# Performance work log

Measured on AMD Instinct MI355X. Metric: run time of the kernel, lower is better.

The kernel has to match this reference:

```python
import jax, jax.numpy as jnp
import numpy as np

D_MODEL = 768
N_HEAD = 8
D_K = D_MODEL // N_HEAD
SCALE = float(np.sqrt(D_K))
NEG = -1e9


def setup_inputs() -> dict:
    key = jax.random.key(0)
    ks = jax.random.split(key, 8)
    B, S = 2, 2048
    q = jax.random.normal(ks[0], (B, S, D_MODEL), dtype=jnp.float32)
    k = jax.random.normal(ks[1], (B, S, D_MODEL), dtype=jnp.float32)
    v = jax.random.normal(ks[2], (B, S, D_MODEL), dtype=jnp.float32)
    mask = jax.random.randint(ks[3], (B, 1, S, S), 0, 2, dtype=jnp.int32)
    # nn.Linear(d, d, bias=False) weights, stored as [in, out] for x @ W
    init = 1.0 / np.sqrt(D_MODEL)
    Wq = jax.random.uniform(ks[4], (D_MODEL, D_MODEL), jnp.float32, -init, init)
    Wk = jax.random.uniform(ks[5], (D_MODEL, D_MODEL), jnp.float32, -init, init)
    Wv = jax.random.uniform(ks[6], (D_MODEL, D_MODEL), jnp.float32, -init, init)
    Wo = jax.random.uniform(ks[7], (D_MODEL, D_MODEL), jnp.float32, -init, init)
    return {"query": q, "key": k, "value": v, "mask": mask,
            "Wq": Wq, "Wk": Wk, "Wv": Wv, "Wo": Wo}


def _split_heads(x):
    B, S, _ = x.shape
    return x.reshape(B, S, N_HEAD, D_K).transpose(0, 2, 1, 3)  # [B,H,S,Dk]


def reference(query, key, value, mask, Wq, Wk, Wv, Wo):
    Q = _split_heads(query @ Wq)
    K = _split_heads(key @ Wk)
    V = _split_heads(value @ Wv)
    logits = jnp.einsum('bhqd,bhkd->bhqk', Q, K) / SCALE  # [B,H,S,S]
    logits = jnp.where(mask == 0, NEG, logits)
    attn = jax.nn.softmax(logits, axis=-1)
    x = jnp.einsum('bhqk,bhkd->bhqd', attn, V)  # dropout=0 (eval)
    B, H, S, Dk = x.shape
    concat = x.transpose(0, 2, 1, 3).reshape(B, S, H * Dk)
    return concat @ Wo, attn
```

## Files before the change

### kernel.cpp

```cpp
#include <hip/hip_runtime.h>
#include <hip/hip_bf16.h>

typedef __bf16 bf16_t;
typedef __bf16 bf16x4 __attribute__((ext_vector_type(4)));
typedef __bf16 bf16x8 __attribute__((ext_vector_type(8)));
typedef float f32x4 __attribute__((ext_vector_type(4)));

#define MFMA16(a, b, c) __builtin_amdgcn_mfma_f32_16x16x32_bf16(a, b, c, 0, 0, 0)

constexpr int B_ = 2, S_ = 2048, DM = 768, H_ = 8, DK = 96;
constexpr size_t OUT_ELEMS = 3145728;
constexpr float INV_SCALE = 0.10206207261596575f;
constexpr float NEGINF = -1e9f;


__global__ __launch_bounds__(256) void prep_w(const float* __restrict__ w0,
                                              const float* __restrict__ w1,
                                              const float* __restrict__ w2,
                                              const float* __restrict__ w3,
                                              bf16_t* __restrict__ wt) {
    __shared__ float tile[32][33];
    const int z = blockIdx.z;
    const float* W = (z == 0) ? w0 : (z == 1) ? w1 : (z == 2) ? w2 : w3;
    bf16_t* out = wt + (size_t)z * DM * DM;
    const int k0 = blockIdx.x * 32, n0 = blockIdx.y * 32;
    const int tx = threadIdx.x & 31, ty = threadIdx.x >> 5;
#pragma unroll
    for (int i = 0; i < 32; i += 8) tile[ty + i][tx] = W[(size_t)(k0 + ty + i) * DM + n0 + tx];
    __syncthreads();
#pragma unroll
    for (int i = 0; i < 32; i += 8) out[(size_t)(n0 + ty + i) * DM + k0 + tx] = (bf16_t)tile[tx][ty + i];
}

template <int AMODE>
__device__ __forceinline__ void gemm_core(const void* __restrict__ Aglob,
                                          const bf16_t* __restrict__ Bt,
                                          int gm0, int gn0, f32x4 acc[4][4]) {
    __shared__ bf16_t As[128][40];
    __shared__ bf16_t Bs[128][40];
    const int tid = threadIdx.x, lane = tid & 63, wid = tid >> 6;
    const int wr = wid >> 1, wc = wid & 1;
    const int l15 = lane & 15, lq = lane >> 4;
    for (int kt = 0; kt < DM / 32; ++kt) {
        if (AMODE == 0) {
            const float* A = (const float*)Aglob;
#pragma unroll
            for (int p = 0; p < 4; ++p) {
                const int row = p * 32 + (tid >> 3);
                const int c4 = (tid & 7) * 4;
                const float4 vv = *(const float4*)&A[(size_t)(gm0 + row) * DM + kt * 32 + c4];
                As[row][c4 + 0] = (bf16_t)vv.x; As[row][c4 + 1] = (bf16_t)vv.y;
                As[row][c4 + 2] = (bf16_t)vv.z; As[row][c4 + 3] = (bf16_t)vv.w;
            }
        } else {
            const bf16_t* A = (const bf16_t*)Aglob;
#pragma unroll
            for (int p = 0; p < 2; ++p) {
                const int row = p * 64 + (tid >> 2);
                const int c8 = (tid & 3) * 8;
                *(uint4*)&As[row][c8] = *(const uint4*)&A[(size_t)(gm0 + row) * DM + kt * 32 + c8];
            }
        }
#pragma unroll
        for (int p = 0; p < 2; ++p) {
            const int row = p * 64 + (tid >> 2);
            const int c8 = (tid & 3) * 8;
            *(uint4*)&Bs[row][c8] = *(const uint4*)&Bt[(size_t)(gn0 + row) * DM + kt * 32 + c8];
        }
        __syncthreads();
        bf16x8 af[4], bfr[4];
#pragma unroll
        for (int i = 0; i < 4; ++i) af[i] = *(const bf16x8*)&As[wr * 64 + i * 16 + l15][lq * 8];
#pragma unroll
        for (int i = 0; i < 4; ++i) bfr[i] = *(const bf16x8*)&Bs[wc * 64 + i * 16 + l15][lq * 8];
#pragma unroll
        for (int i = 0; i < 4; ++i)
#pragma unroll
            for (int j = 0; j < 4; ++j) acc[i][j] = MFMA16(af[i], bfr[j], acc[i][j]);
        __syncthreads();
    }
}

__global__ __launch_bounds__(256) void qkv_gemm(const float* __restrict__ Xq,
                                                const float* __restrict__ Xk,
                                                const float* __restrict__ Xv,
                                                const bf16_t* __restrict__ Wt,
                                                bf16_t* __restrict__ Qw,
                                                bf16_t* __restrict__ Kw,
                                                bf16_t* __restrict__ Vt) {
    const int z = blockIdx.z;
    const float* A = (z == 0) ? Xq : (z == 1) ? Xk : Xv;
    const bf16_t* Bz = Wt + (size_t)z * DM * DM;
    const int gm0 = blockIdx.x * 128, gn0 = blockIdx.y * 128;
    f32x4 acc[4][4];
#pragma unroll
    for (int i = 0; i < 4; ++i)
#pragma unroll
        for (int j = 0; j < 4; ++j) acc[i][j] = (f32x4){0.f, 0.f, 0.f, 0.f};
    gemm_core<0>(A, Bz, gm0, gn0, acc);
    const int lane = threadIdx.x & 63, wid = threadIdx.x >> 6;
    const int wr = wid >> 1, wc = wid & 1;
#pragma unroll
    for (int i = 0; i < 4; ++i)
#pragma unroll
        for (int j = 0; j < 4; ++j)
#pragma unroll
            for (int e = 0; e < 4; ++e) {
                const int gm = gm0 + wr * 64 + i * 16 + (lane >> 4) * 4 + e;
                const int gn = gn0 + wc * 64 + j * 16 + (lane & 15);
                const int b = gm >> 11, s = gm & 2047;
                const int h = gn / DK, dk = gn % DK;
                const float val = acc[i][j][e];
                if (z == 2)
                    Vt[(((size_t)b * H_ + h) * DK + dk) * S_ + s] = (bf16_t)val;
                else {
                    bf16_t* dst = (z == 0) ? Qw : Kw;
                    dst[(((size_t)b * H_ + h) * S_ + s) * DK + dk] = (bf16_t)val;
                }
            }
}

__global__ __launch_bounds__(256, 1) void attn_fused(const bf16_t* __restrict__ Qw,
                                                     const bf16_t* __restrict__ Kw,
                                                     const int* __restrict__ mask,
                                                     const bf16_t* __restrict__ Vt,
                                                     float* __restrict__ attnf,
                                                     bf16_t* __restrict__ Xc) {
    const int bh = blockIdx.y;
    const int q0 = blockIdx.x * 16;
    const int tid = threadIdx.x, lane = tid & 63, w = tid >> 6;
    const int l15 = lane & 15, lq = lane >> 4;
    const int b = bh >> 3, h = bh & 7;

    __shared__ float redmax[4][16];
    __shared__ float redsum[4][16];
    __shared__ bf16_t p_lds[4][16][40];
    __shared__ float pv_part[4][16][96];

    bf16x8 aq[3];
    const bf16_t* qbase = Qw + ((size_t)bh * S_ + q0 + l15) * DK + lq * 8;
#pragma unroll
    for (int kk = 0; kk < 3; ++kk) aq[kk] = *(const bf16x8*)(qbase + kk * 32);

    f32x4 accs[32];
    float rmax = -1e30f;
    const bf16_t* kbase = Kw + (size_t)bh * S_ * DK;
    const int* mrow = mask + ((size_t)b * S_ + q0 + l15) * S_;

#pragma unroll
    for (int t = 0; t < 32; ++t) {
        const int c0 = (w * 32 + t) * 16;
        f32x4 acc = {0.f, 0.f, 0.f, 0.f};
#pragma unroll
        for (int kk = 0; kk < 3; ++kk) {
            bf16x8 kf = *(const bf16x8*)(kbase + (size_t)(c0 + l15) * DK + kk * 32 + lq * 8);
            acc = MFMA16(kf, aq[kk], acc);
        }
        const int4 mk = *(const int4*)(mrow + c0 + lq * 4);
        const int mke[4] = {mk.x, mk.y, mk.z, mk.w};
#pragma unroll
        for (int e = 0; e < 4; ++e) {
            const float lv = (mke[e] == 0) ? NEGINF : acc[e] * INV_SCALE;
            acc[e] = lv;
            rmax = fmaxf(rmax, lv);
        }
        accs[t] = acc;
    }
    rmax = fmaxf(rmax, __shfl_xor(rmax, 16, 64));
    rmax = fmaxf(rmax, __shfl_xor(rmax, 32, 64));
    if (lane < 16) redmax[w][lane] = rmax;
    __syncthreads();
    const float gmax = fmaxf(fmaxf(redmax[0][l15], redmax[1][l15]),
                             fmaxf(redmax[2][l15], redmax[3][l15]));

    float rsum = 0.f;
#pragma unroll
    for (int t = 0; t < 32; ++t) {
#pragma unroll
        for (int e = 0; e < 4; ++e) {
            const float ev = __expf(accs[t][e] - gmax);
            accs[t][e] = ev;
            rsum += ev;
        }
    }
    rsum += __shfl_xor(rsum, 16, 64);
    rsum += __shfl_xor(rsum, 32, 64);
    if (lane < 16) redsum[w][lane] = rsum;
    __syncthreads();
    const float inv = 1.0f / (redsum[0][l15] + redsum[1][l15] + redsum[2][l15] + redsum[3][l15]);

    f32x4 acc6[6];
#pragma unroll
    for (int f = 0; f < 6; ++f) acc6[f] = (f32x4){0.f, 0.f, 0.f, 0.f};
    float* arow = attnf + ((size_t)bh * S_ + q0 + l15) * S_;
    const bf16_t* vbase = Vt + (size_t)bh * DK * S_ + lq * 8;

    for (int u = 0; u < 16; ++u) {
#pragma unroll
        for (int half = 0; half < 2; ++half) {
            const int t = 2 * u + half;
            const int c0 = (w * 32 + t) * 16;
            bf16x4 nb;
#pragma unroll
            for (int e = 0; e < 4; ++e) nb[e] = (bf16_t)(accs[t][e] * inv);
            float4 st;
            st.x = (float)nb[0]; st.y = (float)nb[1]; st.z = (float)nb[2]; st.w = (float)nb[3];
            *(float4*)(arow + c0 + lq * 4) = st;
            *(bf16x4*)&p_lds[w][l15][half * 16 + lq * 4] = nb;
        }
        asm volatile("s_waitcnt lgkmcnt(0)" ::: "memory");
        const bf16x8 pa = *(const bf16x8*)&p_lds[w][l15][lq * 8];
        const int k0 = (w * 512) + u * 32;
#pragma unroll
        for (int f = 0; f < 6; ++f) {
            const bf16x8 vb = *(const bf16x8*)(vbase + (size_t)(f * 16 + l15) * S_ + k0);
            acc6[f] = MFMA16(pa, vb, acc6[f]);
        }
    }

#pragma unroll
    for (int f = 0; f < 6; ++f)
#pragma unroll
        for (int e = 0; e < 4; ++e) pv_part[w][lq * 4 + e][f * 16 + l15] = acc6[f][e];
    __syncthreads();
    for (int i = tid; i < 16 * 96; i += 256) {
        const int row = i / 96, col = i % 96;
        const float s = pv_part[0][row][col] + pv_part[1][row][col] + pv_part[2][row][col] +
                        pv_part[3][row][col];
        Xc[((size_t)b * S_ + q0 + row) * DM + h * DK + col] = (bf16_t)s;
    }
}

__global__ __launch_bounds__(256) void out_gemm(const bf16_t* __restrict__ Xc,
                                                const bf16_t* __restrict__ Wot,
                                                float* __restrict__ outf) {
    const int gm0 = blockIdx.x * 128, gn0 = blockIdx.y * 128;
    f32x4 acc[4][4];
#pragma unroll
    for (int i = 0; i < 4; ++i)
#pragma unroll
        for (int j = 0; j < 4; ++j) acc[i][j] = (f32x4){0.f, 0.f, 0.f, 0.f};
    gemm_core<1>(Xc, Wot, gm0, gn0, acc);
    const int lane = threadIdx.x & 63, wid = threadIdx.x >> 6;
    const int wr = wid >> 1, wc = wid & 1;
#pragma unroll
    for (int i = 0; i < 4; ++i)
#pragma unroll
        for (int j = 0; j < 4; ++j)
#pragma unroll
            for (int e = 0; e < 4; ++e) {
                const int gm = gm0 + wr * 64 + i * 16 + (lane >> 4) * 4 + e;
                const int gn = gn0 + wc * 64 + j * 16 + (lane & 15);
                outf[(size_t)gm * DM + gn] = (float)(bf16_t)acc[i][j][e];
            }
}

extern "C" void kernel_launch(void* const* d_in, const int* in_sizes, int n_in,
                              void* d_out, int out_size, void* d_ws, size_t ws_size,
                              hipStream_t stream) {
    const float* q = (const float*)d_in[0];
    const float* k = (const float*)d_in[1];
    const float* v = (const float*)d_in[2];
    const int* mask = (const int*)d_in[3];
    const float* Wq = (const float*)d_in[4];
    const float* Wk = (const float*)d_in[5];
    const float* Wv = (const float*)d_in[6];
    const float* Wo = (const float*)d_in[7];

    float* outf = (float*)d_out;
    float* attnf = (float*)d_out + OUT_ELEMS;

    char* ws = (char*)d_ws;
    bf16_t* Qw = (bf16_t*)ws;
    bf16_t* Kw = Qw + (size_t)B_ * H_ * S_ * DK;
    bf16_t* Vt = Kw + (size_t)B_ * H_ * S_ * DK;
    bf16_t* Wt = Vt + (size_t)B_ * H_ * S_ * DK;
    bf16_t* Xc = Qw;

    Xc = Wt + (size_t)4 * DM * DM;

    prep_w<<<dim3(24, 24, 4), 256, 0, stream>>>(Wq, Wk, Wv, Wo, Wt);
    qkv_gemm<<<dim3(32, 6, 3), 256, 0, stream>>>(q, k, v, Wt, Qw, Kw, Vt);
    attn_fused<<<dim3(128, 16), 256, 0, stream>>>(Qw, Kw, mask, Vt, attnf, Xc);
    out_gemm<<<dim3(32, 6), 256, 0, stream>>>(Xc, Wt + (size_t)3 * DM * DM, outf);
}
```

Baseline: 260.4 us.

## Pack mask to bits and restructure attention into two-pass online softmax per wave

Result: slower. 316.1 us (+21.4%).

```diff
diff --git a/kernel.cpp b/kernel.cpp
--- a/kernel.cpp
+++ b/kernel.cpp
@@ -5,6 +5,7 @@
 typedef __bf16 bf16x4 __attribute__((ext_vector_type(4)));
 typedef __bf16 bf16x8 __attribute__((ext_vector_type(8)));
 typedef float f32x4 __attribute__((ext_vector_type(4)));
+typedef unsigned long long u64;
 
 #define MFMA16(a, b, c) __builtin_amdgcn_mfma_f32_16x16x32_bf16(a, b, c, 0, 0, 0)
 
@@ -13,6 +14,21 @@
 constexpr float INV_SCALE = 0.10206207261596575f;
 constexpr float NEGINF = -1e9f;
 
+constexpr size_t QW_OFF = 0, KW_OFF = 6291456, VT_OFF = 12582912, WT_OFF = 18874368;
+constexpr size_t XC_OFF = 23592960, MB_OFF = 29884416;
+
+__global__ __launch_bounds__(256) void pack_mask(const int* __restrict__ mask,
+                                                 u64* __restrict__ bits) {
+    const int row = blockIdx.x;
+    const int tid = threadIdx.x, lane = tid & 63, wv = tid >> 6;
+    const int* mrow = mask + (size_t)row * S_;
+    u64* brow = bits + (size_t)row * 32;
+#pragma unroll
+    for (int p = 0; p < 8; ++p) {
+        const u64 b = __ballot(mrow[p * 256 + wv * 64 + lane] != 0);
+        if (lane == 0) brow[p * 4 + wv] = b;
+    }
+}
 
 __global__ __launch_bounds__(256) void prep_w(const float* __restrict__ w0,
                                               const float* __restrict__ w1,
@@ -120,115 +136,146 @@
             }
 }
 
-__global__ __launch_bounds__(256, 1) void attn_fused(const bf16_t* __restrict__ Qw,
+__global__ __launch_bounds__(256, 4) void attn_fused(const bf16_t* __restrict__ Qw,
                                                      const bf16_t* __restrict__ Kw,
-                                                     const int* __restrict__ mask,
+                                                     const u64* __restrict__ mbits,
                                                      const bf16_t* __restrict__ Vt,
                                                      float* __restrict__ attnf,
                                                      bf16_t* __restrict__ Xc) {
     const int bh = blockIdx.y;
-    const int q0 = blockIdx.x * 16;
     const int tid = threadIdx.x, lane = tid & 63, w = tid >> 6;
     const int l15 = lane & 15, lq = lane >> 4;
     const int b = bh >> 3, h = bh & 7;
-
-    __shared__ float redmax[4][16];
-    __shared__ float redsum[4][16];
-    __shared__ bf16_t p_lds[4][16][40];
-    __shared__ float pv_part[4][16][96];
-
-    bf16x8 aq[3];
-    const bf16_t* qbase = Qw + ((size_t)bh * S_ + q0 + l15) * DK + lq * 8;
-#pragma unroll
-    for (int kk = 0; kk < 3; ++kk) aq[kk] = *(const bf16x8*)(qbase + kk * 32);
-
-    f32x4 accs[32];
-    float rmax = -1e30f;
-    const bf16_t* kbase = Kw + (size_t)bh * S_ * DK;
-    const int* mrow = mask + ((size_t)b * S_ + q0 + l15) * S_;
-
-#pragma unroll
-    for (int t = 0; t < 32; ++t) {
-        const int c0 = (w * 32 + t) * 16;
-        f32x4 acc = {0.f, 0.f, 0.f, 0.f};
+    const int qb = blockIdx.x * 128 + w * 32;
+
+    __shared__ bf16_t p_lds[4][2][16][40];
+
+    bf16x8 aq0[3], aq1[3];
+    {
+        const bf16_t* qb0 = Qw + ((size_t)bh * S_ + qb + l15) * DK + lq * 8;
+        const bf16_t* qb1 = qb0 + (size_t)16 * DK;
 #pragma unroll
         for (int kk = 0; kk < 3; ++kk) {
-            bf16x8 kf = *(const bf16x8*)(kbase + (size_t)(c0 + l15) * DK + kk * 32 + lq * 8);
-            acc = MFMA16(kf, aq[kk], acc);
-        }
-        const int4 mk = *(const int4*)(mrow + c0 + lq * 4);
-        const int mke[4] = {mk.x, mk.y, mk.z, mk.w};
+            aq0[kk] = *(const bf16x8*)(qb0 + kk * 32);
+            aq1[kk] = *(const bf16x8*)(qb1 + kk * 32);
+        }
+    }
+    const bf16_t* kbase = Kw + (size_t)bh * S_ * DK + lq * 8;
+    const u64* mb0 = mbits + ((size_t)b * S_ + qb + l15) * 32;
+    const u64* mb1 = mb0 + 16 * 32;
+
+    float m0 = -3e38f, s0 = 0.f, m1 = -3e38f, s1 = 0.f;
+    for (int tg = 0; tg < 32; ++tg) {
+        const u64 w0 = mb0[tg];
+        const u64 w1 = mb1[tg];
+#pragma unroll
+        for (int dt = 0; dt < 4; ++dt) {
+            const int t = tg * 4 + dt;
+            const bf16_t* kr = kbase + (size_t)(t * 16 + l15) * DK;
+            bf16x8 kf0 = *(const bf16x8*)(kr);
+            bf16x8 kf1 = *(const bf16x8*)(kr + 32);
+            bf16x8 kf2 = *(const bf16x8*)(kr + 64);
+            f32x4 a0 = {0.f, 0.f, 0.f, 0.f}, a1 = {0.f, 0.f, 0.f, 0.f};
+            a0 = MFMA16(kf0, aq0[0], a0); a0 = MFMA16(kf1, aq0[1], a0); a0 = MFMA16(kf2, aq0[2], a0);
+            a1 = MFMA16(kf0, aq1[0], a1); a1 = MFMA16(kf1, aq1[1], a1); a1 = MFMA16(kf2, aq1[2], a1);
+            const int sh = dt * 16 + lq * 4;
+            const unsigned b0 = (unsigned)(w0 >> sh) & 0xFu;
+            const unsigned b1 = (unsigned)(w1 >> sh) & 0xFu;
+            float lv0[4], lv1[4];
+#pragma unroll
+            for (int e = 0; e < 4; ++e) {
+                lv0[e] = ((b0 >> e) & 1u) ? a0[e] * INV_SCALE : NEGINF;
+                lv1[e] = ((b1 >> e) & 1u) ? a1[e] * INV_SCALE : NEGINF;
+            }
+            const float tm0 = fmaxf(fmaxf(lv0[0], lv0[1]), fmaxf(lv0[2], lv0[3]));
+            const float tm1 = fmaxf(fmaxf(lv1[0], lv1[1]), fmaxf(lv1[2], lv1[3]));
+            if (tm0 > m0) { s0 *= __expf(m0 - tm0); m0 = tm0; }
+            if (tm1 > m1) { s1 *= __expf(m1 - tm1); m1 = tm1; }
+#pragma unroll
+            for (int e = 0; e < 4; ++e) {
+                s0 += __expf(lv0[e] - m0);
+                s1 += __expf(lv1[e] - m1);
+            }
+        }
+    }
+#pragma unroll
+    for (int off = 16; off <= 32; off <<= 1) {
+        const float om0 = __shfl_xor(m0, off, 64), os0 = __shfl_xor(s0, off, 64);
+        const float om1 = __shfl_xor(m1, off, 64), os1 = __shfl_xor(s1, off, 64);
+        const float nm0 = fmaxf(m0, om0), nm1 = fmaxf(m1, om1);
+        s0 = s0 * __expf(m0 - nm0) + os0 * __expf(om0 - nm0);
+        s1 = s1 * __expf(m1 - nm1) + os1 * __expf(om1 - nm1);
+        m0 = nm0; m1 = nm1;
+    }
+    const float inv0 = 1.0f / s0, inv1 = 1.0f / s1;
+
+    f32x4 acc60[6], acc61[6];
+#pragma unroll
+    for (int f = 0; f < 6; ++f) {
+        acc60[f] = (f32x4){0.f, 0.f, 0.f, 0.f};
+        acc61[f] = (f32x4){0.f, 0.f, 0.f, 0.f};
+    }
+    float* arow0 = attnf + ((size_t)bh * S_ + qb + l15) * S_;
+    float* arow1 = arow0 + (size_t)16 * S_;
+    const bf16_t* vbase = Vt + (size_t)bh * DK * S_ + lq * 8;
+
+    for (int ug = 0; ug < 32; ++ug) {
+        const u64 w0 = mb0[ug];
+        const u64 w1 = mb1[ug];
+#pragma unroll
+        for (int uh = 0; uh < 2; ++uh) {
+            const int u = ug * 2 + uh;
+#pragma unroll
+            for (int half = 0; half < 2; ++half) {
+                const int t = u * 2 + half;
+                const bf16_t* kr = kbase + (size_t)(t * 16 + l15) * DK;
+                bf16x8 kf0 = *(const bf16x8*)(kr);
+                bf16x8 kf1 = *(const bf16x8*)(kr + 32);
+                bf16x8 kf2 = *(const bf16x8*)(kr + 64);
+                f32x4 a0 = {0.f, 0.f, 0.f, 0.f}, a1 = {0.f, 0.f, 0.f, 0.f};
+                a0 = MFMA16(kf0, aq0[0], a0); a0 = MFMA16(kf1, aq0[1], a0); a0 = MFMA16(kf2, aq0[2], a0);
+                a1 = MFMA16(kf0, aq1[0], a1); a1 = MFMA16(kf1, aq1[1], a1); a1 = MFMA16(kf2, aq1[2], a1);
+                const int sh = (uh * 2 + half) * 16 + lq * 4;
+                const unsigned b0 = (unsigned)(w0 >> sh) & 0xFu;
+                const unsigned b1 = (unsigned)(w1 >> sh) & 0xFu;
+                bf16x4 nb0, nb1;
+#pragma unroll
+                for (int e = 0; e < 4; ++e) {
+                    const float lv0 = ((b0 >> e) & 1u) ? a0[e] * INV_SCALE : NEGINF;
+                    const float lv1 = ((b1 >> e) & 1u) ? a1[e] * INV_SCALE : NEGINF;
+                    nb0[e] = (bf16_t)(__expf(lv0 - m0) * inv0);
+                    nb1[e] = (bf16_t)(__expf(lv1 - m1) * inv1);
+                }
+                float4 st0, st1;
+                st0.x = (float)nb0[0]; st0.y = (float)nb0[1]; st0.z = (float)nb0[2]; st0.w = (float)nb0[3];
+                st1.x = (float)nb1[0]; st1.y = (float)nb1[1]; st1.z = (float)nb1[2]; st1.w = (float)nb1[3];
+                *(float4*)(arow0 + t * 16 + lq * 4) = st0;
+                *(float4*)(arow1 + t * 16 + lq * 4) = st1;
+                *(bf16x4*)&p_lds[w][0][l15][half * 16 + lq * 4] = nb0;
+                *(bf16x4*)&p_lds[w][1][l15][half * 16 + lq * 4] = nb1;
+            }
+            asm volatile("s_waitcnt lgkmcnt(0)" ::: "memory");
+            const bf16x8 pa0 = *(const bf16x8*)&p_lds[w][0][l15][lq * 8];
+            const bf16x8 pa1 = *(const bf16x8*)&p_lds[w][1][l15][lq * 8];
+            const int k0 = u * 32;
+#pragma unroll
+            for (int f = 0; f < 6; ++f) {
+                const bf16x8 vb = *(const bf16x8*)(vbase + (size_t)(f * 16 + l15) * S_ + k0);
+                acc60[f] = MFMA16(pa0, vb, acc60[f]);
+                acc61[f] = MFMA16(pa1, vb, acc61[f]);
+            }
+        }
+    }
+
+#pragma unroll
+    for (int f = 0; f < 6; ++f)
 #pragma unroll
         for (int e = 0; e < 4; ++e) {
-            const float lv = (mke[e] == 0) ? NEGINF : acc[e] * INV_SCALE;
-            acc[e] = lv;
-            rmax = fmaxf(rmax, lv);
-        }
-        accs[t] = acc;
-    }
-    rmax = fmaxf(rmax, __shfl_xor(rmax, 16, 64));
-    rmax = fmaxf(rmax, __shfl_xor(rmax, 32, 64));
-    if (lane < 16) redmax[w][lane] = rmax;
-    __syncthreads();
-    const float gmax = fmaxf(fmaxf(redmax[0][l15], redmax[1][l15]),
-                             fmaxf(redmax[2][l15], redmax[3][l15]));
-
-    float rsum = 0.f;
-#pragma unroll
-    for (int t = 0; t < 32; ++t) {
-#pragma unroll
-        for (int e = 0; e < 4; ++e) {
-            const float ev = __expf(accs[t][e] - gmax);
-            accs[t][e] = ev;
-            rsum += ev;
-        }
-    }
-    rsum += __shfl_xor(rsum, 16, 64);
-    rsum += __shfl_xor(rsum, 32, 64);
-    if (lane < 16) redsum[w][lane] = rsum;
-    __syncthreads();
-    const float inv = 1.0f / (redsum[0][l15] + redsum[1][l15] + redsum[2][l15] + redsum[3][l15]);
-
-    f32x4 acc6[6];
-#pragma unroll
-    for (int f = 0; f < 6; ++f) acc6[f] = (f32x4){0.f, 0.f, 0.f, 0.f};
-    float* arow = attnf + ((size_t)bh * S_ + q0 + l15) * S_;
-    const bf16_t* vbase = Vt + (size_t)bh * DK * S_ + lq * 8;
-
-    for (int u = 0; u < 16; ++u) {
-#pragma unroll
-        for (int half = 0; half < 2; ++half) {
-            const int t = 2 * u + half;
-            const int c0 = (w * 32 + t) * 16;
-            bf16x4 nb;
-#pragma unroll
-            for (int e = 0; e < 4; ++e) nb[e] = (bf16_t)(accs[t][e] * inv);
-            float4 st;
-            st.x = (float)nb[0]; st.y = (float)nb[1]; st.z = (float)nb[2]; st.w = (float)nb[3];
-            *(float4*)(arow + c0 + lq * 4) = st;
-            *(bf16x4*)&p_lds[w][l15][half * 16 + lq * 4] = nb;
-        }
-        asm volatile("s_waitcnt lgkmcnt(0)" ::: "memory");
-        const bf16x8 pa = *(const bf16x8*)&p_lds[w][l15][lq * 8];
-        const int k0 = (w * 512) + u * 32;
-#pragma unroll
-        for (int f = 0; f < 6; ++f) {
-            const bf16x8 vb = *(const bf16x8*)(vbase + (size_t)(f * 16 + l15) * S_ + k0);
-            acc6[f] = MFMA16(pa, vb, acc6[f]);
-        }
-    }
-
-#pragma unroll
-    for (int f = 0; f < 6; ++f)
-#pragma unroll
-        for (int e = 0; e < 4; ++e) pv_part[w][lq * 4 + e][f * 16 + l15] = acc6[f][e];
-    __syncthreads();
-    for (int i = tid; i < 16 * 96; i += 256) {
-        const int row = i / 96, col = i % 96;
-        const float s = pv_part[0][row][col] + pv_part[1][row][col] + pv_part[2][row][col] +
-                        pv_part[3][row][col];
-        Xc[((size_t)b * S_ + q0 + row) * DM + h * DK + col] = (bf16_t)s;
-    }
+            const int col = h * DK + f * 16 + l15;
+            const int q0r = qb + lq * 4 + e;
+            Xc[((size_t)b * S_ + q0r) * DM + col] = (bf16_t)acc60[f][e];
+            Xc[((size_t)b * S_ + q0r + 16) * DM + col] = (bf16_t)acc61[f][e];
+        }
 }
 
 __global__ __launch_bounds__(256) void out_gemm(const bf16_t* __restrict__ Xc,
@@ -271,16 +318,16 @@
     float* attnf = (float*)d_out + OUT_ELEMS;
 
     char* ws = (char*)d_ws;
-    bf16_t* Qw = (bf16_t*)ws;
-    bf16_t* Kw = Qw + (size_t)B_ * H_ * S_ * DK;
-    bf16_t* Vt = Kw + (size_t)B_ * H_ * S_ * DK;
-    bf16_t* Wt = Vt + (size_t)B_ * H_ * S_ * DK;
-    bf16_t* Xc = Qw;
-
-    Xc = Wt + (size_t)4 * DM * DM;
+    bf16_t* Qw = (bf16_t*)(ws + QW_OFF);
+    bf16_t* Kw = (bf16_t*)(ws + KW_OFF);
+    bf16_t* Vt = (bf16_t*)(ws + VT_OFF);
+    bf16_t* Wt = (bf16_t*)(ws + WT_OFF);
+    bf16_t* Xc = (bf16_t*)(ws + XC_OFF);
+    u64* mbits = (u64*)(ws + MB_OFF);
 
     prep_w<<<dim3(24, 24, 4), 256, 0, stream>>>(Wq, Wk, Wv, Wo, Wt);
+    pack_mask<<<B_ * S_, 256, 0, stream>>>(mask, mbits);
     qkv_gemm<<<dim3(32, 6, 3), 256, 0, stream>>>(q, k, v, Wt, Qw, Kw, Vt);
-    attn_fused<<<dim3(128, 16), 256, 0, stream>>>(Qw, Kw, mask, Vt, attnf, Xc);
+    attn_fused<<<dim3(16, 16), 256, 0, stream>>>(Qw, Kw, mbits, Vt, attnf, Xc);
     out_gemm<<<dim3(32, 6), 256, 0, stream>>>(Xc, Wt + (size_t)3 * DM * DM, outf);
 }
```

## Pack mask into bitmask once and widen attention blocks to eight waves

Applied to the files above, without the earlier changes.

Result: faster. 248.5 us (-4.6%).

```diff
diff --git a/kernel.cpp b/kernel.cpp
--- a/kernel.cpp
+++ b/kernel.cpp
@@ -5,6 +5,7 @@
 typedef __bf16 bf16x4 __attribute__((ext_vector_type(4)));
 typedef __bf16 bf16x8 __attribute__((ext_vector_type(8)));
 typedef float f32x4 __attribute__((ext_vector_type(4)));
+typedef unsigned long long u64;
 
 #define MFMA16(a, b, c) __builtin_amdgcn_mfma_f32_16x16x32_bf16(a, b, c, 0, 0, 0)
 
@@ -13,6 +14,21 @@
 constexpr float INV_SCALE = 0.10206207261596575f;
 constexpr float NEGINF = -1e9f;
 
+constexpr size_t QW_OFF = 0, KW_OFF = 6291456, VT_OFF = 12582912, WT_OFF = 18874368;
+constexpr size_t XC_OFF = 23592960, MB_OFF = 29884416;
+
+__global__ __launch_bounds__(256) void pack_mask(const int* __restrict__ mask,
+                                                 u64* __restrict__ bits) {
+    const int row = blockIdx.x;
+    const int tid = threadIdx.x, lane = tid & 63, wv = tid >> 6;
+    const int* mrow = mask + (size_t)row * S_;
+    u64* brow = bits + (size_t)row * 32;
+#pragma unroll
+    for (int p = 0; p < 8; ++p) {
+        const u64 b = __ballot(mrow[p * 256 + wv * 64 + lane] != 0);
+        if (lane == 0) brow[p * 4 + wv] = b;
+    }
+}
 
 __global__ __launch_bounds__(256) void prep_w(const float* __restrict__ w0,
                                               const float* __restrict__ w1,
@@ -120,9 +136,9 @@
             }
 }
 
-__global__ __launch_bounds__(256, 1) void attn_fused(const bf16_t* __restrict__ Qw,
+__global__ __launch_bounds__(512, 4) void attn_fused(const bf16_t* __restrict__ Qw,
                                                      const bf16_t* __restrict__ Kw,
-                                                     const int* __restrict__ mask,
+                                                     const u64* __restrict__ mbits,
                                                      const bf16_t* __restrict__ Vt,
                                                      float* __restrict__ attnf,
                                                      bf16_t* __restrict__ Xc) {
@@ -132,85 +148,93 @@
     const int l15 = lane & 15, lq = lane >> 4;
     const int b = bh >> 3, h = bh & 7;
 
-    __shared__ float redmax[4][16];
-    __shared__ float redsum[4][16];
-    __shared__ bf16_t p_lds[4][16][40];
-    __shared__ float pv_part[4][16][96];
+    __shared__ float redmax[8][16];
+    __shared__ float redsum[8][16];
+    __shared__ bf16_t p_lds[8][16][40];
+    __shared__ float pv_part[8][16][96];
 
     bf16x8 aq[3];
-    const bf16_t* qbase = Qw + ((size_t)bh * S_ + q0 + l15) * DK + lq * 8;
-#pragma unroll
-    for (int kk = 0; kk < 3; ++kk) aq[kk] = *(const bf16x8*)(qbase + kk * 32);
-
-    f32x4 accs[32];
+    {
+        const bf16_t* qb = Qw + ((size_t)bh * S_ + q0 + l15) * DK + lq * 8;
+#pragma unroll
+        for (int kk = 0; kk < 3; ++kk) aq[kk] = *(const bf16x8*)(qb + kk * 32);
+    }
+    const bf16_t* kbase = Kw + (size_t)bh * S_ * DK + lq * 8;
+    const u64* mb = mbits + ((size_t)b * S_ + q0 + l15) * 32;
+
+    f32x4 accs[16];
     float rmax = -1e30f;
-    const bf16_t* kbase = Kw + (size_t)bh * S_ * DK;
-    const int* mrow = mask + ((size_t)b * S_ + q0 + l15) * S_;
-
-#pragma unroll
-    for (int t = 0; t < 32; ++t) {
-        const int c0 = (w * 32 + t) * 16;
-        f32x4 acc = {0.f, 0.f, 0.f, 0.f};
-#pragma unroll
-        for (int kk = 0; kk < 3; ++kk) {
-            bf16x8 kf = *(const bf16x8*)(kbase + (size_t)(c0 + l15) * DK + kk * 32 + lq * 8);
-            acc = MFMA16(kf, aq[kk], acc);
-        }
-        const int4 mk = *(const int4*)(mrow + c0 + lq * 4);
-        const int mke[4] = {mk.x, mk.y, mk.z, mk.w};
-#pragma unroll
-        for (int e = 0; e < 4; ++e) {
-            const float lv = (mke[e] == 0) ? NEGINF : acc[e] * INV_SCALE;
-            acc[e] = lv;
-            rmax = fmaxf(rmax, lv);
-        }
-        accs[t] = acc;
+#pragma unroll
+    for (int tg = 0; tg < 4; ++tg) {
+        const u64 mw = mb[w * 4 + tg];
+#pragma unroll
+        for (int dt = 0; dt < 4; ++dt) {
+            const int t = tg * 4 + dt;
+            const int kt = w * 16 + t;
+            const bf16_t* kr = kbase + (size_t)(kt * 16 + l15) * DK;
+            f32x4 acc = {0.f, 0.f, 0.f, 0.f};
+            acc = MFMA16(*(const bf16x8*)(kr), aq[0], acc);
+            acc = MFMA16(*(const bf16x8*)(kr + 32), aq[1], acc);
+            acc = MFMA16(*(const bf16x8*)(kr + 64), aq[2], acc);
+            const int sh = dt * 16 + lq * 4;
+            const unsigned bm = (unsigned)(mw >> sh) & 0xFu;
+#pragma unroll
+            for (int e = 0; e < 4; ++e) {
+                const float lv = ((bm >> e) & 1u) ? acc[e] * INV_SCALE : NEGINF;
+                acc[e] = lv;
+                rmax = fmaxf(rmax, lv);
+            }
+            accs[t] = acc;
+        }
     }
     rmax = fmaxf(rmax, __shfl_xor(rmax, 16, 64));
     rmax = fmaxf(rmax, __shfl_xor(rmax, 32, 64));
     if (lane < 16) redmax[w][lane] = rmax;
     __syncthreads();
-    const float gmax = fmaxf(fmaxf(redmax[0][l15], redmax[1][l15]),
-                             fmaxf(redmax[2][l15], redmax[3][l15]));
+    float gmax = redmax[0][l15];
+#pragma unroll
+    for (int i = 1; i < 8; ++i) gmax = fmaxf(gmax, redmax[i][l15]);
 
     float rsum = 0.f;
 #pragma unroll
-    for (int t = 0; t < 32; ++t) {
+    for (int t = 0; t < 16; ++t)
 #pragma unroll
         for (int e = 0; e < 4; ++e) {
             const float ev = __expf(accs[t][e] - gmax);
             accs[t][e] = ev;
             rsum += ev;
         }
-    }
     rsum += __shfl_xor(rsum, 16, 64);
     rsum += __shfl_xor(rsum, 32, 64);
     if (lane < 16) redsum[w][lane] = rsum;
     __syncthreads();
-    const float inv = 1.0f / (redsum[0][l15] + redsum[1][l15] + redsum[2][l15] + redsum[3][l15]);
+    float ssum = redsum[0][l15];
+#pragma unroll
+    for (int i = 1; i < 8; ++i) ssum += redsum[i][l15];
+    const float inv = 1.0f / ssum;
 
     f32x4 acc6[6];
 #pragma unroll
     for (int f = 0; f < 6; ++f) acc6[f] = (f32x4){0.f, 0.f, 0.f, 0.f};
-    float* arow = attnf + ((size_t)bh * S_ + q0 + l15) * S_;
+    float* arow = attnf + ((size_t)bh * S_ + q0 + l15) * S_ + w * 256;
     const bf16_t* vbase = Vt + (size_t)bh * DK * S_ + lq * 8;
 
-    for (int u = 0; u < 16; ++u) {
+#pragma unroll
+    for (int u = 0; u < 8; ++u) {
 #pragma unroll
         for (int half = 0; half < 2; ++half) {
             const int t = 2 * u + half;
-            const int c0 = (w * 32 + t) * 16;
             bf16x4 nb;
 #pragma unroll
             for (int e = 0; e < 4; ++e) nb[e] = (bf16_t)(accs[t][e] * inv);
             float4 st;
             st.x = (float)nb[0]; st.y = (float)nb[1]; st.z = (float)nb[2]; st.w = (float)nb[3];
-            *(float4*)(arow + c0 + lq * 4) = st;
+            *(float4*)(arow + t * 16 + lq * 4) = st;
             *(bf16x4*)&p_lds[w][l15][half * 16 + lq * 4] = nb;
         }
         asm volatile("s_waitcnt lgkmcnt(0)" ::: "memory");
         const bf16x8 pa = *(const bf16x8*)&p_lds[w][l15][lq * 8];
-        const int k0 = (w * 512) + u * 32;
+        const int k0 = w * 256 + u * 32;
 #pragma unroll
         for (int f = 0; f < 6; ++f) {
             const bf16x8 vb = *(const bf16x8*)(vbase + (size_t)(f * 16 + l15) * S_ + k0);
@@ -223,10 +247,11 @@
 #pragma unroll
         for (int e = 0; e < 4; ++e) pv_part[w][lq * 4 + e][f * 16 + l15] = acc6[f][e];
     __syncthreads();
-    for (int i = tid; i < 16 * 96; i += 256) {
+    for (int i = tid; i < 16 * 96; i += 512) {
         const int row = i / 96, col = i % 96;
-        const float s = pv_part[0][row][col] + pv_part[1][row][col] + pv_part[2][row][col] +
-                        pv_part[3][row][col];
+        float s = pv_part[0][row][col];
+#pragma unroll
+        for (int j = 1; j < 8; ++j) s += pv_part[j][row][col];
         Xc[((size_t)b * S_ + q0 + row) * DM + h * DK + col] = (bf16_t)s;
     }
 }
@@ -271,16 +296,16 @@
     float* attnf = (float*)d_out + OUT_ELEMS;
 
     char* ws = (char*)d_ws;
-    bf16_t* Qw = (bf16_t*)ws;
-    bf16_t* Kw = Qw + (size_t)B_ * H_ * S_ * DK;
-    bf16_t* Vt = Kw + (size_t)B_ * H_ * S_ * DK;
-    bf16_t* Wt = Vt + (size_t)B_ * H_ * S_ * DK;
-    bf16_t* Xc = Qw;
-
-    Xc = Wt + (size_t)4 * DM * DM;
+    bf16_t* Qw = (bf16_t*)(ws + QW_OFF);
+    bf16_t* Kw = (bf16_t*)(ws + KW_OFF);
+    bf16_t* Vt = (bf16_t*)(ws + VT_OFF);
+    bf16_t* Wt = (bf16_t*)(ws + WT_OFF);
+    bf16_t* Xc = (bf16_t*)(ws + XC_OFF);
+    u64* mbits = (u64*)(ws + MB_OFF);
 
     prep_w<<<dim3(24, 24, 4), 256, 0, stream>>>(Wq, Wk, Wv, Wo, Wt);
+    pack_mask<<<B_ * S_, 256, 0, stream>>>(mask, mbits);
     qkv_gemm<<<dim3(32, 6, 3), 256, 0, stream>>>(q, k, v, Wt, Qw, Kw, Vt);
-    attn_fused<<<dim3(128, 16), 256, 0, stream>>>(Qw, Kw, mask, Vt, attnf, Xc);
+    attn_fused<<<dim3(128, 16), 512, 0, stream>>>(Qw, Kw, mbits, Vt, attnf, Xc);
     out_gemm<<<dim3(32, 6), 256, 0, stream>>>(Xc, Wt + (size_t)3 * DM * DM, outf);
 }
```
